# Performance work log

Measured on AMD Instinct MI355X. Metric: run time of the kernel, lower is better.

## Reference

```python
import jax, jax.numpy as jnp
import numpy as np

DIM = 384
HEADS = 12
WS = 7
SHIFT = 3
MLP_HID = 1536
EPS = 1e-5


def layer_norm(x, w, b):
    m = x.mean(-1, keepdims=True)
    v = ((x - m) ** 2).mean(-1, keepdims=True)
    return (x - m) / jnp.sqrt(v + EPS) * w + b


def setup_inputs() -> dict:
    key = jax.random.key(0)
    ks = jax.random.split(key, 8)
    B, H, W, C = 32, 56, 56, DIM
    s = 0.02
    return {
        "x": jax.random.normal(ks[0], (B, H * W, C), jnp.float32),
        "H": H,
        "W": W,
        "norm1_w": jnp.ones((C,), jnp.float32),
        "norm1_b": jnp.zeros((C,), jnp.float32),
        "qkv_w": jax.random.normal(ks[1], (3 * C, C), jnp.float32) * s,
        "qkv_b": jnp.zeros((3 * C,), jnp.float32),
        "out_w": jax.random.normal(ks[2], (C, C), jnp.float32) * s,
        "out_b": jnp.zeros((C,), jnp.float32),
        "norm2_w": jnp.ones((C,), jnp.float32),
        "norm2_b": jnp.zeros((C,), jnp.float32),
        "fc1_w": jax.random.normal(ks[3], (MLP_HID, C), jnp.float32) * s,
        "fc1_b": jnp.zeros((MLP_HID,), jnp.float32),
        "fc2_w": jax.random.normal(ks[4], (C, MLP_HID), jnp.float32) * s,
        "fc2_b": jnp.zeros((C,), jnp.float32),
    }


def reference(x, H, W, norm1_w, norm1_b, qkv_w, qkv_b, out_w, out_b,
              norm2_w, norm2_b, fc1_w, fc1_b, fc2_w, fc2_b):
    B, L, C = x.shape
    shortcut = x
    h = layer_norm(x, norm1_w, norm1_b).reshape(B, H, W, C)
    if SHIFT > 0:
        h = jnp.roll(h, (-SHIFT, -SHIFT), axis=(1, 2))
    # window partition (pad to multiple of WS; static since H, W are Python ints)
    pad_h = (WS - H % WS) % WS
    pad_w = (WS - W % WS) % WS
    if pad_h or pad_w:
        h = jnp.pad(h, ((0, 0), (0, pad_h), (0, pad_w), (0, 0)))
    Hp, Wp = H + pad_h, W + pad_w
    S = WS * WS
    win = h.reshape(B, Hp // WS, WS, Wp // WS, WS, C)
    win = win.transpose(0, 1, 3, 2, 4, 5).reshape(-1, S, C)  # (nW*B, S, C)
    # windowed multi-head self-attention (torch nn.MultiheadAttention math)
    hd = C // HEADS
    scale = 1.0 / np.sqrt(hd)
    qkv = win @ qkv_w.T + qkv_b  # (N, S, 3C)
    q, k, v = jnp.split(qkv, 3, axis=-1)
    to_heads = lambda t: t.reshape(-1, S, HEADS, hd).transpose(0, 2, 1, 3)
    q, k, v = to_heads(q), to_heads(k), to_heads(v)
    attn = jax.nn.softmax(jnp.einsum('nhsd,nhtd->nhst', q, k) * scale, axis=-1)
    o = jnp.einsum('nhst,nhtd->nhsd', attn, v)
    o = o.transpose(0, 2, 1, 3).reshape(-1, S, C) @ out_w.T + out_b
    # window reverse
    o = o.reshape(B, Hp // WS, Wp // WS, WS, WS, C)
    o = o.transpose(0, 1, 3, 2, 4, 5).reshape(B, Hp, Wp, C)
    if pad_h or pad_w:
        o = o[:, :H, :W, :]
    if SHIFT > 0:
        o = jnp.roll(o, (SHIFT, SHIFT), axis=(1, 2))
    x2 = shortcut + o.reshape(B, L, C)
    h2 = layer_norm(x2, norm2_w, norm2_b)
    mlp = jax.nn.gelu(h2 @ fc1_w.T + fc1_b, approximate=False) @ fc2_w.T + fc2_b
    return x2 + mlp
```

## Files before the change

kernel.cpp:

```cpp
#include <hip/hip_runtime.h>
#include <hip/hip_bf16.h>
#include <math.h>

#define TOKENS   100352
#define CDIM     384
#define SEQ      49
#define NHEADS   12
#define HDIM     32
#define QKVD     1152
#define HIDD     1536
#define IMG      56

typedef __attribute__((ext_vector_type(8))) short  short8;
typedef __attribute__((ext_vector_type(4))) float  f32x4;

__device__ __forceinline__ int token_to_pixel(int m) {
    int w  = m / SEQ, s = m % SEQ;
    int b  = w >> 6, wr = w & 63;
    int wy = wr >> 3, wx = wr & 7;
    int sy = s / 7,  sx = s % 7;
    int y = wy * 7 + sy + 3; if (y >= IMG) y -= IMG;
    int x = wx * 7 + sx + 3; if (x >= IMG) x -= IMG;
    return b * (IMG * IMG) + y * IMG + x;
}

__device__ __forceinline__ void split2(float v, __hip_bfloat16& hi, __hip_bfloat16& lo) {
    hi = __float2bfloat16(v);
    lo = __float2bfloat16(v - __bfloat162float(hi));
}

__device__ __forceinline__ void gload16(const void* g, void* l) {
    __builtin_amdgcn_global_load_lds((const __attribute__((address_space(1))) void*)g,
                                     (__attribute__((address_space(3))) void*)l, 16, 0, 0);
}

template<int WINDOWED>
__global__ __launch_bounds__(128)
void ln_pack_kernel(const float* __restrict__ in, const float* __restrict__ w,
                    const float* __restrict__ b, __hip_bfloat16* __restrict__ out,
                    int mbase)
{
    const int ml  = blockIdx.x;
    const int src = WINDOWED ? token_to_pixel(mbase + ml) : ml;
    const float* row = in + (size_t)src * CDIM;
    const int t = threadIdx.x;

    float v0 = row[t], v1 = row[t + 128], v2 = row[t + 256];
    float s  = v0 + v1 + v2;
    float ss = fmaf(v0, v0, fmaf(v1, v1, v2 * v2));
    #pragma unroll
    for (int off = 1; off < 64; off <<= 1) {
        s  += __shfl_xor(s,  off, 64);
        ss += __shfl_xor(ss, off, 64);
    }
    __shared__ float l1[2], l2[2];
    if ((t & 63) == 0) { l1[t >> 6] = s; l2[t >> 6] = ss; }
    __syncthreads();
    float S  = l1[0] + l1[1];
    float SS = l2[0] + l2[1];
    float mean = S * (1.0f / CDIM);
    float var  = SS * (1.0f / CDIM) - mean * mean;
    float rstd = rsqrtf(var + 1e-5f);

    __hip_bfloat16* orow = out + (size_t)ml * (2 * CDIM);
    #pragma unroll
    for (int q = 0; q < 3; ++q) {
        int c = t + q * 128;
        float v = (q == 0 ? v0 : q == 1 ? v1 : v2);
        float y = (v - mean) * rstd * w[c] + b[c];
        split2(y, orow[c], orow[CDIM + c]);
    }
}

__global__ __launch_bounds__(256)
void pack_w_kernel(const float* __restrict__ W, __hip_bfloat16* __restrict__ Wp,
                   int N, int K)
{
    const int total = N * K;
    for (int i = blockIdx.x * 256 + threadIdx.x; i < total; i += gridDim.x * 256) {
        int n = i / K, k = i % K;
        split2(W[i], Wp[(size_t)n * 2 * K + k], Wp[(size_t)n * 2 * K + K + k]);
    }
}

template<int MODE>
__global__ __launch_bounds__(256)
void gemm_bf16x3(const __hip_bfloat16* __restrict__ A2,
                 const __hip_bfloat16* __restrict__ B2,
                 const float* __restrict__ bias, const float* resid,
                 void* Cout, int M, int N, int K, int mbase)
{
    __shared__ __align__(16) unsigned short Ah[128 * 32];
    __shared__ __align__(16) unsigned short Al[128 * 32];
    __shared__ __align__(16) unsigned short Bh[128 * 32];
    __shared__ __align__(16) unsigned short Bl[128 * 32];

    const int tid  = threadIdx.x;
    const int wave = tid >> 6, lane = tid & 63;

    const int nwg  = gridDim.x * gridDim.y;
    const int orig = blockIdx.y * gridDim.x + blockIdx.x;
    const int qc   = nwg >> 3, rc = nwg & 7;
    const int xcd  = orig & 7, off = orig >> 3;
    const int lin  = ((xcd < rc) ? xcd * (qc + 1) : rc * (qc + 1) + (xcd - rc) * qc) + off;
    const int m0 = (lin / gridDim.x) * 128, n0 = (lin % gridDim.x) * 128;

    const int srow = wave * 16 + (lane >> 2);
    const int scol = ((lane & 3) ^ ((lane >> 3) & 3)) * 8;
    const size_t K2 = (size_t)2 * K;
    const __hip_bfloat16* gA0 = A2 + (size_t)(m0 + srow) * K2 + scol;
    const __hip_bfloat16* gB0 = B2 + (size_t)(n0 + srow) * K2 + scol;
    const size_t rstep = (size_t)64 * K2;
    unsigned short* lAh0 = &Ah[(wave * 16) * 32];
    unsigned short* lAh1 = &Ah[(64 + wave * 16) * 32];
    unsigned short* lAl0 = &Al[(wave * 16) * 32];
    unsigned short* lAl1 = &Al[(64 + wave * 16) * 32];
    unsigned short* lBh0 = &Bh[(wave * 16) * 32];
    unsigned short* lBh1 = &Bh[(64 + wave * 16) * 32];
    unsigned short* lBl0 = &Bl[(wave * 16) * 32];
    unsigned short* lBl1 = &Bl[(64 + wave * 16) * 32];

    const int wm = (wave >> 1) * 64, wn = (wave & 1) * 64;
    const int fr = lane & 15;
    const int sa = (((lane >> 4) ^ ((fr >> 1) & 3)) * 8);

    f32x4 acc[4][4];
    #pragma unroll
    for (int i = 0; i < 4; ++i)
        #pragma unroll
        for (int j = 0; j < 4; ++j) acc[i][j] = {0.f, 0.f, 0.f, 0.f};

    for (int k0 = 0; k0 < K; k0 += 32) {
        const __hip_bfloat16* a = gA0 + k0;
        const __hip_bfloat16* b = gB0 + k0;
        gload16(a,             lAh0);  gload16(a + rstep,     lAh1);
        gload16(a + K,         lAl0);  gload16(a + K + rstep, lAl1);
        gload16(b,             lBh0);  gload16(b + rstep,     lBh1);
        gload16(b + K,         lBl0);  gload16(b + K + rstep, lBl1);
        __syncthreads();

        short8 ah[4], al[4], bh[4], bl[4];
        #pragma unroll
        for (int f = 0; f < 4; ++f) {
            const int ra = (wm + f * 16 + fr) * 32 + sa;
            const int rb = (wn + f * 16 + fr) * 32 + sa;
            ah[f] = *(const short8*)&Ah[ra];
            al[f] = *(const short8*)&Al[ra];
            bh[f] = *(const short8*)&Bh[rb];
            bl[f] = *(const short8*)&Bl[rb];
        }
        #pragma unroll
        for (int i = 0; i < 4; ++i)
            #pragma unroll
            for (int j = 0; j < 4; ++j) {
                acc[i][j] = __builtin_amdgcn_mfma_f32_16x16x32_bf16(ah[i], bh[j], acc[i][j], 0, 0, 0);
                acc[i][j] = __builtin_amdgcn_mfma_f32_16x16x32_bf16(al[i], bh[j], acc[i][j], 0, 0, 0);
                acc[i][j] = __builtin_amdgcn_mfma_f32_16x16x32_bf16(ah[i], bl[j], acc[i][j], 0, 0, 0);
            }
        __syncthreads();
    }

    const int colb = n0 + wn + fr;
    const int rowb = m0 + wm + (lane >> 4) * 4;
    float bv[4];
    #pragma unroll
    for (int j = 0; j < 4; ++j) bv[j] = bias[colb + j * 16];

    #pragma unroll
    for (int i = 0; i < 4; ++i) {
        #pragma unroll
        for (int r = 0; r < 4; ++r) {
            const int row = rowb + i * 16 + r;
            if constexpr (MODE == 0) {
                float* C = (float*)Cout;
                size_t base = (size_t)row * N;
                #pragma unroll
                for (int j = 0; j < 4; ++j)
                    C[base + colb + j * 16] = acc[i][j][r] + bv[j];
            } else if constexpr (MODE == 1) {
                float* C = (float*)Cout;
                size_t base = (size_t)token_to_pixel(mbase + row) * CDIM;
                #pragma unroll
                for (int j = 0; j < 4; ++j) {
                    size_t idx = base + colb + j * 16;
                    C[idx] = resid[idx] + acc[i][j][r] + bv[j];
                }
            } else if constexpr (MODE == 2) {
                __hip_bfloat16* Cb = (__hip_bfloat16*)Cout;
                size_t base = (size_t)row * (2 * N);
                #pragma unroll
                for (int j = 0; j < 4; ++j) {
                    float v = acc[i][j][r] + bv[j];
                    float g = 0.5f * v * (1.0f + erff(v * 0.70710678118654752f));
                    split2(g, Cb[base + colb + j * 16], Cb[base + N + colb + j * 16]);
                }
            } else {
                float* C = (float*)Cout;
                size_t base = (size_t)row * N;
                #pragma unroll
                for (int j = 0; j < 4; ++j) {
                    size_t idx = base + colb + j * 16;
                    C[idx] = resid[idx] + acc[i][j][r] + bv[j];
                }
            }
        }
    }
}

__global__ __launch_bounds__(256)
void attn_kernel(const float* __restrict__ qkv, __hip_bfloat16* __restrict__ o2)
{
    const int blk = blockIdx.x;
    const int w   = blk / NHEADS;
    const int h   = blk % NHEADS;
    const int tid = threadIdx.x;

    __shared__ float qs[SEQ][33], ks[SEQ][33], vs[SEQ][36];
    __shared__ float ps[SEQ][50];
    __shared__ float rmax[SEQ], rsum[SEQ];

    const size_t base = (size_t)w * SEQ * QKVD + h * HDIM;
    for (int i = tid; i < SEQ * HDIM; i += 256) {
        int s = i >> 5, d = i & 31;
        size_t g = base + (size_t)s * QKVD + d;
        qs[s][d] = qkv[g];
        ks[s][d] = qkv[g + CDIM];
        vs[s][d] = qkv[g + 2 * CDIM];
    }
    __syncthreads();

    const float scale = 0.17677669529663687f;
    for (int it = tid; it < SEQ * 7; it += 256) {
        int r = it / 7, cg = (it % 7) * 7;
        float a[7] = {0, 0, 0, 0, 0, 0, 0};
        for (int kk = 0; kk < HDIM; ++kk) {
            float qv = qs[r][kk];
            #pragma unroll
            for (int j = 0; j < 7; ++j) a[j] = fmaf(qv, ks[cg + j][kk], a[j]);
        }
        #pragma unroll
        for (int j = 0; j < 7; ++j) ps[r][cg + j] = a[j] * scale;
    }
    __syncthreads();
    if (tid < SEQ) {
        float m = -1e30f;
        for (int c = 0; c < SEQ; ++c) m = fmaxf(m, ps[tid][c]);
        rmax[tid] = m;
    }
    __syncthreads();
    for (int e = tid; e < SEQ * SEQ; e += 256) {
        int r = e / SEQ, c = e % SEQ;
        ps[r][c] = __expf(ps[r][c] - rmax[r]);
    }
    __syncthreads();
    if (tid < SEQ) {
        float s = 0.f;
        for (int c = 0; c < SEQ; ++c) s += ps[tid][c];
        rsum[tid] = 1.0f / s;
    }
    __syncthreads();
    for (int it = tid; it < SEQ * 4; it += 256) {
        int s = it >> 2, dg = (it & 3) * 8;
        float a[8] = {0, 0, 0, 0, 0, 0, 0, 0};
        for (int t = 0; t < SEQ; ++t) {
            float pv = ps[s][t];
            #pragma unroll
            for (int j = 0; j < 8; ++j) a[j] = fmaf(pv, vs[t][dg + j], a[j]);
        }
        float inv = rsum[s];
        __hip_bfloat16 hv[8], lv[8];
        #pragma unroll
        for (int j = 0; j < 8; ++j) split2(a[j] * inv, hv[j], lv[j]);
        size_t r = ((size_t)w * SEQ + s) * (2 * CDIM) + h * HDIM + dg;
        *(short8*)&o2[r]        = *(short8*)hv;
        *(short8*)&o2[r + CDIM] = *(short8*)lv;
    }
}

extern "C" void kernel_launch(void* const* d_in, const int* in_sizes, int n_in,
                              void* d_out, int out_size, void* d_ws, size_t ws_size,
                              hipStream_t stream)
{
    const float* x    = (const float*)d_in[0];
    const float* n1w  = (const float*)d_in[3];
    const float* n1b  = (const float*)d_in[4];
    const float* qkvw = (const float*)d_in[5];
    const float* qkvb = (const float*)d_in[6];
    const float* outw = (const float*)d_in[7];
    const float* outb = (const float*)d_in[8];
    const float* n2w  = (const float*)d_in[9];
    const float* n2b  = (const float*)d_in[10];
    const float* fc1w = (const float*)d_in[11];
    const float* fc1b = (const float*)d_in[12];
    const float* fc2w = (const float*)d_in[13];
    const float* fc2b = (const float*)d_in[14];
    float* out = (float*)d_out;

    const size_t WBYTES = 7077888;
    char* wsb = (char*)d_ws;
    __hip_bfloat16* wq  = (__hip_bfloat16*)wsb;
    __hip_bfloat16* wo  = wq  + 884736;
    __hip_bfloat16* wf1 = wo  + 294912;
    __hip_bfloat16* wf2 = wf1 + 1179648;
    char* R = wsb + WBYTES;

    int rows = 6272;
    const int cand[5] = {100352, 50176, 25088, 12544, 6272};
    for (int i = 0; i < 5; ++i)
        if (WBYTES + (size_t)cand[i] * 7680 <= ws_size) { rows = cand[i]; break; }
    const int nch = TOKENS / rows;

    __hip_bfloat16* win_b = (__hip_bfloat16*)R;
    float*          qkv_b = (float*)(R + (size_t)rows * 1536);
    __hip_bfloat16* o_b   = (__hip_bfloat16*)(R + (size_t)rows * 6144);
    __hip_bfloat16* h2_b  = (__hip_bfloat16*)R;
    __hip_bfloat16* hid_b = (__hip_bfloat16*)(R + (size_t)rows * 1536);

    pack_w_kernel<<<1728, 256, 0, stream>>>(qkvw, wq,  QKVD, CDIM);
    pack_w_kernel<<<576,  256, 0, stream>>>(outw, wo,  CDIM, CDIM);
    pack_w_kernel<<<2304, 256, 0, stream>>>(fc1w, wf1, HIDD, CDIM);
    pack_w_kernel<<<2304, 256, 0, stream>>>(fc2w, wf2, CDIM, HIDD);

    for (int c = 0; c < nch; ++c) {
        const int mb = c * rows;
        ln_pack_kernel<1><<<rows, 128, 0, stream>>>(x, n1w, n1b, win_b, mb);
        gemm_bf16x3<0><<<dim3(QKVD / 128, rows / 128), 256, 0, stream>>>(
            win_b, wq, qkvb, nullptr, qkv_b, rows, QKVD, CDIM, 0);
        attn_kernel<<<(rows / SEQ) * NHEADS, 256, 0, stream>>>(qkv_b, o_b);
        gemm_bf16x3<1><<<dim3(CDIM / 128, rows / 128), 256, 0, stream>>>(
            o_b, wo, outb, x, out, rows, CDIM, CDIM, mb);
    }
    for (int c = 0; c < nch; ++c) {
        const int mb = c * rows;
        float* oc = out + (size_t)mb * CDIM;
        ln_pack_kernel<0><<<rows, 128, 0, stream>>>(oc, n2w, n2b, h2_b, 0);
        gemm_bf16x3<2><<<dim3(HIDD / 128, rows / 128), 256, 0, stream>>>(
            h2_b, wf1, fc1b, nullptr, hid_b, rows, HIDD, CDIM, 0);
        gemm_bf16x3<3><<<dim3(CDIM / 128, rows / 128), 256, 0, stream>>>(
            hid_b, wf2, fc2b, oc, oc, rows, CDIM, HIDD, 0);
    }
}
```

Measured before the change: 2.406 ms.

## Double-buffer GEMM LDS, add tile swizzle, size chunks to workspace

```diff
diff --git a/kernel.cpp b/kernel.cpp
--- a/kernel.cpp
+++ b/kernel.cpp
@@ -88,22 +88,31 @@
 void gemm_bf16x3(const __hip_bfloat16* __restrict__ A2,
                  const __hip_bfloat16* __restrict__ B2,
                  const float* __restrict__ bias, const float* resid,
-                 void* Cout, int M, int N, int K, int mbase)
-{
-    __shared__ __align__(16) unsigned short Ah[128 * 32];
-    __shared__ __align__(16) unsigned short Al[128 * 32];
-    __shared__ __align__(16) unsigned short Bh[128 * 32];
-    __shared__ __align__(16) unsigned short Bl[128 * 32];
+                 void* Cout, int M, int N, int K, int mbase, int SH_, int SW_)
+{
+    __shared__ __align__(16) unsigned short Ah[2][4096];
+    __shared__ __align__(16) unsigned short Al[2][4096];
+    __shared__ __align__(16) unsigned short Bh[2][4096];
+    __shared__ __align__(16) unsigned short Bl[2][4096];
 
     const int tid  = threadIdx.x;
     const int wave = tid >> 6, lane = tid & 63;
 
     const int nwg  = gridDim.x * gridDim.y;
     const int orig = blockIdx.y * gridDim.x + blockIdx.x;
-    const int qc   = nwg >> 3, rc = nwg & 7;
+    const int qc   = nwg >> 3, r8 = nwg & 7;
     const int xcd  = orig & 7, off = orig >> 3;
-    const int lin  = ((xcd < rc) ? xcd * (qc + 1) : rc * (qc + 1) + (xcd - rc) * qc) + off;
-    const int m0 = (lin / gridDim.x) * 128, n0 = (lin % gridDim.x) * 128;
+    const int lin  = ((xcd < r8) ? xcd * (qc + 1) : r8 * (qc + 1) + (xcd - r8) * qc) + off;
+
+    const int gx = gridDim.x, gy = gridDim.y;
+    const int band  = lin / (SH_ * gx);
+    const int sh    = min(SH_, gy - band * SH_);
+    const int rr    = lin - band * SH_ * gx;
+    const int strip = rr / (sh * SW_);
+    const int sw    = min(SW_, gx - strip * SW_);
+    const int r2    = rr - strip * sh * SW_;
+    const int m0 = (band * SH_ + r2 / sw) * 128;
+    const int n0 = (strip * SW_ + r2 % sw) * 128;
 
     const int srow = wave * 16 + (lane >> 2);
     const int scol = ((lane & 3) ^ ((lane >> 3) & 3)) * 8;
@@ -111,14 +120,17 @@
     const __hip_bfloat16* gA0 = A2 + (size_t)(m0 + srow) * K2 + scol;
     const __hip_bfloat16* gB0 = B2 + (size_t)(n0 + srow) * K2 + scol;
     const size_t rstep = (size_t)64 * K2;
-    unsigned short* lAh0 = &Ah[(wave * 16) * 32];
-    unsigned short* lAh1 = &Ah[(64 + wave * 16) * 32];
-    unsigned short* lAl0 = &Al[(wave * 16) * 32];
-    unsigned short* lAl1 = &Al[(64 + wave * 16) * 32];
-    unsigned short* lBh0 = &Bh[(wave * 16) * 32];
-    unsigned short* lBh1 = &Bh[(64 + wave * 16) * 32];
-    unsigned short* lBl0 = &Bl[(wave * 16) * 32];
-    unsigned short* lBl1 = &Bl[(64 + wave * 16) * 32];
+    const int lA0 = (wave * 16) * 32;
+    const int lA1 = (64 + wave * 16) * 32;
+
+#define STAGE(k0, s) do {                                                     \
+        const __hip_bfloat16* a_ = gA0 + (k0);                                \
+        const __hip_bfloat16* b_ = gB0 + (k0);                                \
+        gload16(a_,             &Ah[s][lA0]); gload16(a_ + rstep,     &Ah[s][lA1]); \
+        gload16(a_ + K,         &Al[s][lA0]); gload16(a_ + K + rstep, &Al[s][lA1]); \
+        gload16(b_,             &Bh[s][lA0]); gload16(b_ + rstep,     &Bh[s][lA1]); \
+        gload16(b_ + K,         &Bl[s][lA0]); gload16(b_ + K + rstep, &Bl[s][lA1]); \
+    } while (0)
 
     const int wm = (wave >> 1) * 64, wn = (wave & 1) * 64;
     const int fr = lane & 15;
@@ -130,24 +142,23 @@
         #pragma unroll
         for (int j = 0; j < 4; ++j) acc[i][j] = {0.f, 0.f, 0.f, 0.f};
 
-    for (int k0 = 0; k0 < K; k0 += 32) {
-        const __hip_bfloat16* a = gA0 + k0;
-        const __hip_bfloat16* b = gB0 + k0;
-        gload16(a,             lAh0);  gload16(a + rstep,     lAh1);
-        gload16(a + K,         lAl0);  gload16(a + K + rstep, lAl1);
-        gload16(b,             lBh0);  gload16(b + rstep,     lBh1);
-        gload16(b + K,         lBl0);  gload16(b + K + rstep, lBl1);
-        __syncthreads();
+    const int ksteps = K >> 5;
+    STAGE(0, 0);
+    __syncthreads();
+    int cur = 0;
+    for (int t = 0; t < ksteps; ++t) {
+        const int nxt = cur ^ 1;
+        if (t + 1 < ksteps) STAGE((t + 1) << 5, nxt);
 
         short8 ah[4], al[4], bh[4], bl[4];
         #pragma unroll
         for (int f = 0; f < 4; ++f) {
             const int ra = (wm + f * 16 + fr) * 32 + sa;
             const int rb = (wn + f * 16 + fr) * 32 + sa;
-            ah[f] = *(const short8*)&Ah[ra];
-            al[f] = *(const short8*)&Al[ra];
-            bh[f] = *(const short8*)&Bh[rb];
-            bl[f] = *(const short8*)&Bl[rb];
+            ah[f] = *(const short8*)&Ah[cur][ra];
+            al[f] = *(const short8*)&Al[cur][ra];
+            bh[f] = *(const short8*)&Bh[cur][rb];
+            bl[f] = *(const short8*)&Bl[cur][rb];
         }
         #pragma unroll
         for (int i = 0; i < 4; ++i)
@@ -158,7 +169,9 @@
                 acc[i][j] = __builtin_amdgcn_mfma_f32_16x16x32_bf16(ah[i], bl[j], acc[i][j], 0, 0, 0);
             }
         __syncthreads();
-    }
+        cur = nxt;
+    }
+#undef STAGE
 
     const int colb = n0 + wn + fr;
     const int rowb = m0 + wm + (lane >> 4) * 4;
@@ -303,40 +316,43 @@
     __hip_bfloat16* wf1 = wo  + 294912;
     __hip_bfloat16* wf2 = wf1 + 1179648;
     char* R = wsb + WBYTES;
-
-    int rows = 6272;
-    const int cand[5] = {100352, 50176, 25088, 12544, 6272};
-    for (int i = 0; i < 5; ++i)
-        if (WBYTES + (size_t)cand[i] * 7680 <= ws_size) { rows = cand[i]; break; }
-    const int nch = TOKENS / rows;
-
-    __hip_bfloat16* win_b = (__hip_bfloat16*)R;
-    float*          qkv_b = (float*)(R + (size_t)rows * 1536);
-    __hip_bfloat16* o_b   = (__hip_bfloat16*)(R + (size_t)rows * 6144);
-    __hip_bfloat16* h2_b  = (__hip_bfloat16*)R;
-    __hip_bfloat16* hid_b = (__hip_bfloat16*)(R + (size_t)rows * 1536);
+    const size_t avail = ws_size - WBYTES;
+
+    int r1 = 6272;
+    while (r1 < TOKENS && (size_t)(r1 + 6272) * 6144 <= avail) r1 += 6272;
+    int r2 = 128;
+    while (r2 < TOKENS && (size_t)(r2 + 128) * 7680 <= avail) r2 += 128;
 
     pack_w_kernel<<<1728, 256, 0, stream>>>(qkvw, wq,  QKVD, CDIM);
     pack_w_kernel<<<576,  256, 0, stream>>>(outw, wo,  CDIM, CDIM);
     pack_w_kernel<<<2304, 256, 0, stream>>>(fc1w, wf1, HIDD, CDIM);
     pack_w_kernel<<<2304, 256, 0, stream>>>(fc2w, wf2, CDIM, HIDD);
 
-    for (int c = 0; c < nch; ++c) {
-        const int mb = c * rows;
-        ln_pack_kernel<1><<<rows, 128, 0, stream>>>(x, n1w, n1b, win_b, mb);
-        gemm_bf16x3<0><<<dim3(QKVD / 128, rows / 128), 256, 0, stream>>>(
-            win_b, wq, qkvb, nullptr, qkv_b, rows, QKVD, CDIM, 0);
-        attn_kernel<<<(rows / SEQ) * NHEADS, 256, 0, stream>>>(qkv_b, o_b);
-        gemm_bf16x3<1><<<dim3(CDIM / 128, rows / 128), 256, 0, stream>>>(
-            o_b, wo, outb, x, out, rows, CDIM, CDIM, mb);
-    }
-    for (int c = 0; c < nch; ++c) {
-        const int mb = c * rows;
-        float* oc = out + (size_t)mb * CDIM;
-        ln_pack_kernel<0><<<rows, 128, 0, stream>>>(oc, n2w, n2b, h2_b, 0);
-        gemm_bf16x3<2><<<dim3(HIDD / 128, rows / 128), 256, 0, stream>>>(
-            h2_b, wf1, fc1b, nullptr, hid_b, rows, HIDD, CDIM, 0);
-        gemm_bf16x3<3><<<dim3(CDIM / 128, rows / 128), 256, 0, stream>>>(
-            hid_b, wf2, fc2b, oc, oc, rows, CDIM, HIDD, 0);
-    }
-}
+    {
+        __hip_bfloat16* win_b = (__hip_bfloat16*)R;
+        float*          qkv_b = (float*)(R + (size_t)r1 * 1536);
+        __hip_bfloat16* o_b   = win_b;
+        for (int mb = 0; mb < TOKENS; mb += r1) {
+            const int rc = min(r1, TOKENS - mb);
+            ln_pack_kernel<1><<<rc, 128, 0, stream>>>(x, n1w, n1b, win_b, mb);
+            gemm_bf16x3<0><<<dim3(QKVD / 128, rc / 128), 256, 0, stream>>>(
+                win_b, wq, qkvb, nullptr, qkv_b, rc, QKVD, CDIM, 0, 4, 9);
+            attn_kernel<<<(rc / SEQ) * NHEADS, 256, 0, stream>>>(qkv_b, o_b);
+            gemm_bf16x3<1><<<dim3(CDIM / 128, rc / 128), 256, 0, stream>>>(
+                o_b, wo, outb, x, out, rc, CDIM, CDIM, mb, 8, 3);
+        }
+    }
+    {
+        __hip_bfloat16* h2_b  = (__hip_bfloat16*)R;
+        __hip_bfloat16* hid_b = (__hip_bfloat16*)(R + (size_t)r2 * 1536);
+        for (int mb = 0; mb < TOKENS; mb += r2) {
+            const int rc = min(r2, TOKENS - mb);
+            float* oc = out + (size_t)mb * CDIM;
+            ln_pack_kernel<0><<<rc, 128, 0, stream>>>(oc, n2w, n2b, h2_b, 0);
+            gemm_bf16x3<2><<<dim3(HIDD / 128, rc / 128), 256, 0, stream>>>(
+                h2_b, wf1, fc1b, nullptr, hid_b, rc, HIDD, CDIM, 0, 4, 12);
+            gemm_bf16x3<3><<<dim3(CDIM / 128, rc / 128), 256, 0, stream>>>(
+                hid_b, wf2, fc2b, oc, oc, rc, CDIM, HIDD, 0, 2, 3);
+        }
+    }
+}
```

Result: faster. 2.278 ms (-5.3%).
